# Kernel optimization log

Hardware: AMD Instinct MI355X
Metric: run time of the kernel (lower is better)

Reference implementation:

```python
import math
import jax, jax.numpy as jnp
import numpy as np

DIM = 1280
NUM_HEADS = 16
HEAD_DIM = DIM // NUM_HEADS  # 80
SEQ = 3072


def setup_inputs() -> dict:
    key = jax.random.key(0)
    k1, k2, k3, k4, k5, k6 = jax.random.split(key, 6)
    hidden_states = jax.random.normal(k1, (SEQ, DIM), dtype=jnp.float32)
    # 4 packed images of 768 patches each
    cu_seqlens = jnp.array([0, 768, 1536, 2304, 3072], dtype=jnp.int32)
    rotary_pos_emb = jax.random.normal(k2, (SEQ, HEAD_DIM // 2), dtype=jnp.float32)
    scale = 1.0 / math.sqrt(DIM)
    qkv_w = jax.random.normal(k3, (DIM, 3 * DIM), dtype=jnp.float32) * scale
    qkv_b = jax.random.normal(k4, (3 * DIM,), dtype=jnp.float32) * 0.01
    proj_w = jax.random.normal(k5, (DIM, DIM), dtype=jnp.float32) * scale
    proj_b = jax.random.normal(k6, (DIM,), dtype=jnp.float32) * 0.01
    return {"hidden_states": hidden_states, "cu_seqlens": cu_seqlens,
            "rotary_pos_emb": rotary_pos_emb, "qkv_w": qkv_w, "qkv_b": qkv_b,
            "proj_w": proj_w, "proj_b": proj_b}


def _rotate_half(x):
    half = x.shape[-1] // 2
    return jnp.concatenate([-x[..., half:], x[..., :half]], axis=-1)


def _apply_rope(t, freqs):
    # t: [S, H, hd], freqs: [S, hd//2]
    cos = jnp.cos(freqs)
    sin = jnp.sin(freqs)
    cos = jnp.concatenate([cos, cos], axis=-1)[:, None, :]  # [S,1,hd] (repeat(1,1,2) tiles)
    sin = jnp.concatenate([sin, sin], axis=-1)[:, None, :]
    return (t.astype(jnp.float32) * cos + _rotate_half(t.astype(jnp.float32)) * sin).astype(t.dtype)


def reference(hidden_states, cu_seqlens, rotary_pos_emb, qkv_w, qkv_b, proj_w, proj_b):
    S = hidden_states.shape[0]
    qkv = hidden_states @ qkv_w + qkv_b                      # [S, 3*dim]
    qkv = qkv.reshape(S, 3, NUM_HEADS, HEAD_DIM)
    q, k, v = qkv[:, 0], qkv[:, 1], qkv[:, 2]                # [S, H, hd]
    q = _apply_rope(q, rotary_pos_emb)
    k = _apply_rope(k, rotary_pos_emb)

    # block-diagonal mask from cu_seqlens: positions in the same segment attend
    pos = jnp.arange(S)
    seg = jnp.searchsorted(cu_seqlens, pos, side='right')    # segment id per token
    neg = jnp.finfo(q.dtype).min
    mask = jnp.where(seg[:, None] == seg[None, :], 0.0, neg).astype(q.dtype)  # [S,S]

    qh = q.transpose(1, 0, 2)                                # [H,S,hd]
    kh = k.transpose(1, 0, 2)
    vh = v.transpose(1, 0, 2)
    scores = jnp.einsum('hqd,hkd->hqk', qh, kh) / math.sqrt(HEAD_DIM)
    scores = scores + mask[None]
    attn = jax.nn.softmax(scores.astype(jnp.float32), axis=-1).astype(q.dtype)
    out = jnp.einsum('hqk,hkd->hqd', attn, vh)               # [H,S,hd]
    out = out.transpose(1, 0, 2).reshape(S, DIM)
    return out @ proj_w + proj_b
```

## Files before the change

### kernel.cpp

```cpp
#include <hip/hip_runtime.h>
#include <hip/hip_bf16.h>
#include <math.h>

#define SEQ   3072
#define DIM   1280
#define NH    16
#define HD    80
#define QKV_N 3840

typedef unsigned short u16;
typedef unsigned int   u32;
typedef __attribute__((ext_vector_type(8))) short short8;
typedef __attribute__((ext_vector_type(4))) short short4v;
typedef __attribute__((ext_vector_type(4))) float f32x4;

#if defined(__has_builtin)
#  if __has_builtin(__builtin_amdgcn_mfma_f32_16x16x16bf16_1k)
#    define MFMA16(a,b,c) __builtin_amdgcn_mfma_f32_16x16x16bf16_1k(a,b,c,0,0,0)
#  endif
#endif
#ifndef MFMA16
__device__ __forceinline__ f32x4 mfma16_asm(short4v a, short4v b, f32x4 c) {
    f32x4 d;
    asm volatile("v_mfma_f32_16x16x16_bf16 %0, %1, %2, %3"
                 : "=v"(d) : "v"(a), "v"(b), "0"(c));
    return d;
}
#  define MFMA16(a,b,c) mfma16_asm(a,b,c)
#endif

__device__ __forceinline__ u16 f32_to_bf16(float x) {
    unsigned xb = __float_as_uint(x);
    return (u16)((xb + 0x7fffu + ((xb >> 16) & 1u)) >> 16);
}
__device__ __forceinline__ void split1(float x, u16& h, u16& l) {
    h = f32_to_bf16(x);
    float hf = __uint_as_float(((unsigned)h) << 16);
    l = f32_to_bf16(x - hf);
}
__device__ __forceinline__ u32 pack2(float a, float b) {
    return (u32)f32_to_bf16(a) | ((u32)f32_to_bf16(b) << 16);
}

__device__ __forceinline__ void gload16(const void* g, void* l) {
    __builtin_amdgcn_global_load_lds(
        (const __attribute__((address_space(1))) void*)g,
        (__attribute__((address_space(3))) void*)l, 16, 0, 0);
}

__global__ __launch_bounds__(256) void split_rows(const float* __restrict__ in,
                                                  u16* __restrict__ oh,
                                                  u16* __restrict__ ol, int n4) {
    int i = blockIdx.x * 256 + threadIdx.x;
    int stride = gridDim.x * 256;
    for (; i < n4; i += stride) {
        float4 v = ((const float4*)in)[i];
        ushort4 h, l;
        split1(v.x, h.x, l.x); split1(v.y, h.y, l.y);
        split1(v.z, h.z, l.z); split1(v.w, h.w, l.w);
        ((ushort4*)oh)[i] = h; ((ushort4*)ol)[i] = l;
    }
}

__global__ __launch_bounds__(256) void transpose_w(const float* __restrict__ in,
                                                   u16* __restrict__ o,
                                                   int K, int N) {
    __shared__ float t[32][33];
    const int n0 = blockIdx.x * 32, k0 = blockIdx.y * 32;
    const int tx = threadIdx.x & 31, ty = threadIdx.x >> 5;
    #pragma unroll
    for (int j = 0; j < 4; j++)
        t[ty + j * 8][tx] = in[(size_t)(k0 + ty + j * 8) * N + n0 + tx];
    __syncthreads();
    #pragma unroll
    for (int j = 0; j < 4; j++)
        o[(size_t)(n0 + ty + j * 8) * K + k0 + tx] = f32_to_bf16(t[tx][ty + j * 8]);
}

__global__ __launch_bounds__(256) void gemm_bf16x2(const u16* __restrict__ Ah,
                                                   const u16* __restrict__ Al,
                                                   const u16* __restrict__ Bh,
                                                   const float* __restrict__ bias,
                                                   float* __restrict__ Cf, int ldc,
                                                   u16* __restrict__ Ch,
                                                   u16* __restrict__ Cl, int nsplit,
                                                   int nbn,
                                                   int M, int N, int K) {
    __shared__ u16 lds[2][12288];
    const int tid  = threadIdx.x;
    const int lane = tid & 63;
    const int w    = tid >> 6;

    const int nwg = gridDim.x;
    const int qd  = nwg >> 3, rm = nwg & 7;
    const int xcd = blockIdx.x & 7, idx = blockIdx.x >> 3;
    const int wg  = (xcd < rm ? xcd * (qd + 1) : rm * (qd + 1) + (xcd - rm) * qd) + idx;
    const int bm = wg / nbn, bn = wg - bm * nbn;
    const int wm = w >> 1, wn = w & 1;

    const int rl   = lane >> 2;
    const int slot = lane & 3;
    const int ks   = (slot ^ ((rl >> 1) & 3)) * 8;

    const u16* pbase[3] = { Ah + (size_t)(bm * 128) * K,
                            Al + (size_t)(bm * 128) * K,
                            Bh + (size_t)(bn * 128) * K };
    const u16* csrc[6];
    int cdst[6];
    #pragma unroll
    for (int i = 0; i < 6; i++) {
        int c = w * 6 + i, p = c >> 3, seg = c & 7;
        csrc[i] = pbase[p] + (size_t)(seg * 16 + rl) * K + ks;
        cdst[i] = p * 4096 + seg * 512;
    }

    const f32x4 zero = {0.f, 0.f, 0.f, 0.f};
    f32x4 acc[4][4];
    #pragma unroll
    for (int i = 0; i < 4; i++)
        #pragma unroll
        for (int j = 0; j < 4; j++) acc[i][j] = zero;

    const int r16 = lane & 15, kg = lane >> 4;
    const int sw  = (kg ^ ((r16 >> 1) & 3)) * 16;

    const int nt = K >> 5;

    #pragma unroll
    for (int i = 0; i < 6; i++)
        gload16(csrc[i], &lds[0][cdst[i]]);
    __syncthreads();

    int cur = 0;
    for (int t = 0; t < nt; t++) {
        if (t + 1 < nt) {
            #pragma unroll
            for (int i = 0; i < 6; i++)
                gload16(csrc[i] + (t + 1) * 32, &lds[cur ^ 1][cdst[i]]);
        }

        const char* ldsb = (const char*)&lds[cur][0];
        short8 ah[4], al[4], bh[4];
        #pragma unroll
        for (int i = 0; i < 4; i++) {
            int offA = (wm * 64 + i * 16 + r16) * 64 + sw;
            ah[i] = *(const short8*)(ldsb + offA);
            al[i] = *(const short8*)(ldsb + 8192 + offA);
            int offB = (wn * 64 + i * 16 + r16) * 64 + sw;
            bh[i] = *(const short8*)(ldsb + 16384 + offB);
        }
        #pragma unroll
        for (int i = 0; i < 4; i++)
            #pragma unroll
            for (int j = 0; j < 4; j++) {
                acc[i][j] = __builtin_amdgcn_mfma_f32_16x16x32_bf16(ah[i], bh[j], acc[i][j], 0, 0, 0);
                acc[i][j] = __builtin_amdgcn_mfma_f32_16x16x32_bf16(al[i], bh[j], acc[i][j], 0, 0, 0);
            }

        __syncthreads();
        cur ^= 1;
    }

    const int rg = lane >> 4;
    #pragma unroll
    for (int j = 0; j < 4; j++) {
        int col = bn * 128 + wn * 64 + j * 16 + r16;
        float bv = bias[col];
        #pragma unroll
        for (int i = 0; i < 4; i++) {
            int row0 = bm * 128 + wm * 64 + i * 16 + rg * 4;
            if (col < nsplit) {
                #pragma unroll
                for (int r = 0; r < 4; r++)
                    Cf[(size_t)(row0 + r) * ldc + col] = acc[i][j][r] + bv;
            } else {
                #pragma unroll
                for (int r = 0; r < 4; r++) {
                    float v = acc[i][j][r] + bv;
                    size_t o = (size_t)(row0 + r) * DIM + (col - nsplit);
                    if (Cl) { u16 hh, ll; split1(v, hh, ll); Ch[o] = hh; Cl[o] = ll; }
                    else    { Ch[o] = f32_to_bf16(v); }
                }
            }
        }
    }
}

__global__ __launch_bounds__(256) void rope_split_qk(const float* __restrict__ qk,
                                                     const float* __restrict__ rope,
                                                     u16* __restrict__ Qh, u16* __restrict__ Ql,
                                                     u16* __restrict__ Kh) {
    __shared__ float cs[40], sn[40];
    const int s = blockIdx.x;
    if (threadIdx.x < 40) {
        float f = rope[(size_t)s * 40 + threadIdx.x];
        cs[threadIdx.x] = cosf(f);
        sn[threadIdx.x] = sinf(f);
    }
    __syncthreads();
    const float qs = 0.11180339887498949f;
    const size_t ib = (size_t)s * 2560;
    const size_t ob = (size_t)s * DIM;
    for (int p = threadIdx.x; p < 640; p += 256) {
        int hh = p / 40, j = p - hh * 40;
        float c = cs[j], sv = sn[j];
        int e0 = hh * 80 + j, e1 = e0 + 40;
        float a0 = qk[ib + e0], a1 = qk[ib + e1];
        u16 x, y;
        split1((a0 * c - a1 * sv) * qs, x, y); Qh[ob + e0] = x; Ql[ob + e0] = y;
        split1((a1 * c + a0 * sv) * qs, x, y); Qh[ob + e1] = x; Ql[ob + e1] = y;
        float b0 = qk[ib + 1280 + e0], b1 = qk[ib + 1280 + e1];
        Kh[ob + e0] = f32_to_bf16(b0 * c - b1 * sv);
        Kh[ob + e1] = f32_to_bf16(b1 * c + b0 * sv);
    }
}

__global__ __launch_bounds__(256) void transpose_v(const u16* __restrict__ Vh,
                                                   u16* __restrict__ Vt) {
    __shared__ u16 th[64][88];
    const int hh = blockIdx.x;
    const int s0 = blockIdx.y * 64;
    for (int c = threadIdx.x; c < 640; c += 256) {
        int r = c / 10, cg = c - r * 10;
        *(short8*)&th[r][cg * 8] =
            *(const short8*)(Vh + (size_t)(s0 + r) * DIM + hh * HD + cg * 8);
    }
    __syncthreads();
    for (int c = threadIdx.x; c < 640; c += 256) {
        int d = c >> 3, rg = c & 7;
        short8 v;
        #pragma unroll
        for (int i = 0; i < 8; i++) v[i] = (short)th[rg * 8 + i][d];
        *(short8*)(Vt + (size_t)(hh * HD + d) * SEQ + s0 + rg * 8) = v;
    }
}

__global__ __launch_bounds__(256) void attn_mfma2(const u16* __restrict__ Qh,
                                                  const u16* __restrict__ Ql,
                                                  const u16* __restrict__ Kh,
                                                  const u16* __restrict__ Vt,
                                                  const int* __restrict__ cu,
                                                  u16* __restrict__ Oh,
                                                  u16* __restrict__ Ol) {
    __shared__ u16 lds[2][12288];
    const int tid  = threadIdx.x;
    const int lane = tid & 63;
    const int w    = tid >> 6;
    const int r16  = lane & 15;
    const int kg   = lane >> 4;
    const int h    = blockIdx.x;
    const int q0   = blockIdx.y * 64;

    int kstart, kend;
    {
        int c1 = cu[1], c2 = cu[2], c3 = cu[3];
        if      (q0 < c1) { kstart = cu[0]; kend = c1; }
        else if (q0 < c2) { kstart = c1;    kend = c2; }
        else if (q0 < c3) { kstart = c2;    kend = c3; }
        else              { kstart = c3;    kend = cu[4]; }
    }

    const char* cbase[6];
    int cscale[6];
    #pragma unroll
    for (int i = 0; i < 6; i++) {
        int c = w * 6 + i;
        if (c < 10) {
            int o = c * 1024 + lane * 16;
            int row = o / 160, col = o - row * 160;
            cbase[i]  = (const char*)Kh + (size_t)row * 2560 + h * 160 + col;
            cscale[i] = 2560;
        } else {
            int o = (c - 10) * 1024 + lane * 16;
            int row = o / 160, col = o - row * 160;
            if (row > 79) row = 79;
            cbase[i]  = (const char*)Vt + (size_t)(h * HD + row) * (SEQ * 2) + col;
            cscale[i] = 2;
        }
    }

    const short8 z8 = {0, 0, 0, 0, 0, 0, 0, 0};
    short8 qfh[3], qfl[3];
    {
        const size_t qb = (size_t)(q0 + w * 16 + r16) * DIM + h * HD;
        #pragma unroll
        for (int ks = 0; ks < 3; ks++) {
            int ko = ks * 32 + kg * 8;
            if (ko < HD) {
                qfh[ks] = *(const short8*)(Qh + qb + ko);
                qfl[ks] = *(const short8*)(Ql + qb + ko);
            } else { qfh[ks] = z8; qfl[ks] = z8; }
        }
    }

    const f32x4 zf = {0.f, 0.f, 0.f, 0.f};
    f32x4 acc_o[5] = {zf, zf, zf, zf, zf};
    float m_ = -3.0e38f, l_ = 0.f;

    {
        char* dst = (char*)&lds[0][0] + (w * 6) * 1024;
        #pragma unroll
        for (int i = 0; i < 6; i++)
            gload16(cbase[i] + (size_t)kstart * cscale[i], dst + i * 1024);
    }

    int cur = 0;
    for (int k0 = kstart; k0 < kend; k0 += 64) {
        if (k0 + 64 < kend) {
            char* dst = (char*)&lds[cur ^ 1][0] + (w * 6) * 1024;
            #pragma unroll
            for (int i = 0; i < 6; i++)
                gload16(cbase[i] + (size_t)(k0 + 64) * cscale[i], dst + i * 1024);
            __builtin_amdgcn_sched_barrier(0);
            asm volatile("s_waitcnt vmcnt(6)");
        } else {
            __builtin_amdgcn_sched_barrier(0);
            asm volatile("s_waitcnt vmcnt(0)");
        }
        __builtin_amdgcn_s_barrier();
        __builtin_amdgcn_sched_barrier(0);

        const char* bK = (const char*)&lds[cur][0];
        const char* bV = bK + 10240;

        f32x4 accs[4] = {zf, zf, zf, zf};
        #pragma unroll
        for (int kb = 0; kb < 4; kb++) {
            #pragma unroll
            for (int ks = 0; ks < 3; ks++) {
                short8 af = *(const short8*)(bK + (kb * 16 + r16) * 160 + ks * 64 + kg * 16);
                accs[kb] = __builtin_amdgcn_mfma_f32_16x16x32_bf16(af, qfh[ks], accs[kb], 0, 0, 0);
                accs[kb] = __builtin_amdgcn_mfma_f32_16x16x32_bf16(af, qfl[ks], accs[kb], 0, 0, 0);
            }
        }

        float tmax = -3.0e38f;
        #pragma unroll
        for (int kb = 0; kb < 4; kb++)
            tmax = fmaxf(tmax, fmaxf(fmaxf(accs[kb][0], accs[kb][1]),
                                     fmaxf(accs[kb][2], accs[kb][3])));
        tmax = fmaxf(tmax, __shfl_xor(tmax, 16, 64));
        tmax = fmaxf(tmax, __shfl_xor(tmax, 32, 64));
        float mn = fmaxf(m_, tmax);
        float al = __expf(m_ - mn);
        float lt = 0.f;
        u32 pk[4][2];
        #pragma unroll
        for (int kb = 0; kb < 4; kb++) {
            float p0 = __expf(accs[kb][0] - mn);
            float p1 = __expf(accs[kb][1] - mn);
            float p2 = __expf(accs[kb][2] - mn);
            float p3 = __expf(accs[kb][3] - mn);
            lt += (p0 + p1) + (p2 + p3);
            pk[kb][0] = pack2(p0, p1);
            pk[kb][1] = pack2(p2, p3);
        }
        lt += __shfl_xor(lt, 16, 64);
        lt += __shfl_xor(lt, 32, 64);
        l_ = l_ * al + lt;
        m_ = mn;
        #pragma unroll
        for (int db = 0; db < 5; db++) acc_o[db] *= al;

        #pragma unroll
        for (int kb = 0; kb < 4; kb++) {
            union { u32 u[2]; short4v s; } cv;
            cv.u[0] = pk[kb][0]; cv.u[1] = pk[kb][1];
            short4v pb = cv.s;
            #pragma unroll
            for (int db = 0; db < 5; db++) {
                short4v vf = *(const short4v*)(bV + (db * 16 + r16) * 160 + kb * 32 + kg * 8);
                acc_o[db] = MFMA16(vf, pb, acc_o[db]);
            }
        }

        __builtin_amdgcn_s_barrier();
        __builtin_amdgcn_sched_barrier(0);
        cur ^= 1;
    }

    float inv = 1.0f / l_;
    const size_t ob = (size_t)(q0 + w * 16 + r16) * DIM + h * HD + kg * 4;
    #pragma unroll
    for (int db = 0; db < 5; db++) {
        short4v hv, lv;
        #pragma unroll
        for (int r = 0; r < 4; r++) {
            u16 hh, ll; split1(acc_o[db][r] * inv, hh, ll);
            hv[r] = (short)hh; lv[r] = (short)ll;
        }
        *(short4v*)(Oh + ob + db * 16) = hv;
        *(short4v*)(Ol + ob + db * 16) = lv;
    }
}

__global__ __launch_bounds__(256) void sgemm_bias(const float* __restrict__ A,
                                                  const float* __restrict__ B,
                                                  const float* __restrict__ bias,
                                                  float* __restrict__ C,
                                                  int M, int N, int K) {
    __shared__ float As[8][128];
    __shared__ float Bs[8][128];
    const int tid = threadIdx.x;
    const int tx  = tid & 15;
    const int ty  = tid >> 4;
    const int bx  = blockIdx.x, by = blockIdx.y;
    const int row_a = tid >> 1;
    const int col_a = (tid & 1) * 4;
    const int row_b = tid >> 5;
    const int col_b = (tid & 31) * 4;
    const float* Ap = A + (size_t)(by * 128 + row_a) * K + col_a;
    const float* Bp = B + (size_t)row_b * N + bx * 128 + col_b;
    float acc[8][8];
    #pragma unroll
    for (int i = 0; i < 8; i++)
        #pragma unroll
        for (int j = 0; j < 8; j++) acc[i][j] = 0.f;
    for (int k0 = 0; k0 < K; k0 += 8) {
        float4 av = *(const float4*)(Ap + k0);
        float4 bv = *(const float4*)(Bp + (size_t)k0 * N);
        __syncthreads();
        As[col_a + 0][row_a] = av.x; As[col_a + 1][row_a] = av.y;
        As[col_a + 2][row_a] = av.z; As[col_a + 3][row_a] = av.w;
        *(float4*)&Bs[row_b][col_b] = bv;
        __syncthreads();
        #pragma unroll
        for (int kk = 0; kk < 8; kk++) {
            float a[8], b[8];
            *(float4*)&a[0] = *(const float4*)&As[kk][ty * 8];
            *(float4*)&a[4] = *(const float4*)&As[kk][ty * 8 + 4];
            *(float4*)&b[0] = *(const float4*)&Bs[kk][tx * 8];
            *(float4*)&b[4] = *(const float4*)&Bs[kk][tx * 8 + 4];
            #pragma unroll
            for (int i = 0; i < 8; i++)
                #pragma unroll
                for (int j = 0; j < 8; j++)
                    acc[i][j] = fmaf(a[i], b[j], acc[i][j]);
        }
    }
    const int crow = by * 128 + ty * 8;
    const int ccol = bx * 128 + tx * 8;
    float bs[8];
    #pragma unroll
    for (int j = 0; j < 8; j++) bs[j] = bias[ccol + j];
    #pragma unroll
    for (int i = 0; i < 8; i++) {
        float4 o0, o1;
        o0.x = acc[i][0] + bs[0]; o0.y = acc[i][1] + bs[1];
        o0.z = acc[i][2] + bs[2]; o0.w = acc[i][3] + bs[3];
        o1.x = acc[i][4] + bs[4]; o1.y = acc[i][5] + bs[5];
        o1.z = acc[i][6] + bs[6]; o1.w = acc[i][7] + bs[7];
        *(float4*)(C + (size_t)(crow + i) * N + ccol)     = o0;
        *(float4*)(C + (size_t)(crow + i) * N + ccol + 4) = o1;
    }
}

__global__ __launch_bounds__(256) void rope_kernel(float* __restrict__ qkv,
                                                   const float* __restrict__ rope) {
    const int s = blockIdx.x;
    for (int idx = threadIdx.x; idx < NH * 40; idx += 256) {
        const int hh = idx / 40, j = idx % 40;
        const float f  = rope[(size_t)s * 40 + j];
        const float cs = cosf(f), sn = sinf(f);
        size_t base = (size_t)s * QKV_N + hh * HD;
        float q0 = qkv[base + j], q1 = qkv[base + j + 40];
        qkv[base + j]      = q0 * cs - q1 * sn;
        qkv[base + j + 40] = q1 * cs + q0 * sn;
        size_t kb = base + DIM;
        float k0 = qkv[kb + j], k1 = qkv[kb + j + 40];
        qkv[kb + j]      = k0 * cs - k1 * sn;
        qkv[kb + j + 40] = k1 * cs + k0 * sn;
    }
}

__global__ __launch_bounds__(256) void attn_flash(const float* __restrict__ qkv,
                                                  const int* __restrict__ cu,
                                                  float* __restrict__ aout) {
    __shared__ float Qs[80][68];
    __shared__ float Ks[80][68];
    __shared__ float Vs[64][80];
    float* Ps = &Ks[0][0];
    const int hh  = blockIdx.x;
    const int qt  = blockIdx.y;
    const int tid = threadIdx.x;
    const int tx  = tid & 15;
    const int ty  = tid >> 4;
    const int q0  = qt * 64;
    int c0 = cu[0], c1 = cu[1], c2 = cu[2], c3 = cu[3], c4 = cu[4];
    auto seg = [&](int r, int& s, int& e) {
        if      (r < c1) { s = c0; e = c1; }
        else if (r < c2) { s = c1; e = c2; }
        else if (r < c3) { s = c2; e = c3; }
        else             { s = c3; e = c4; }
    };
    int rs[4], re[4];
    #pragma unroll
    for (int i = 0; i < 4; i++) seg(q0 + ty * 4 + i, rs[i], re[i]);
    int kstart, kend;
    { int s, e; seg(q0, s, e); kstart = s; seg(q0 + 63, s, e); kend = e; }
    for (int i2 = tid; i2 < 64 * 20; i2 += 256) {
        int r = i2 / 20, c4f = (i2 % 20) * 4;
        float4 v = *(const float4*)(qkv + (size_t)(q0 + r) * QKV_N + hh * HD + c4f);
        Qs[c4f + 0][r] = v.x; Qs[c4f + 1][r] = v.y;
        Qs[c4f + 2][r] = v.z; Qs[c4f + 3][r] = v.w;
    }
    float m_[4], l_[4], o_[4][5];
    #pragma unroll
    for (int i = 0; i < 4; i++) {
        m_[i] = -3.0e38f; l_[i] = 0.f;
        #pragma unroll
        for (int d = 0; d < 5; d++) o_[i][d] = 0.f;
    }
    const float scale = 0.11180339887498949f;
    for (int k0 = kstart; k0 < kend; k0 += 64) {
        __syncthreads();
        for (int i2 = tid; i2 < 64 * 20; i2 += 256) {
            int r = i2 / 20, c4f = (i2 % 20) * 4;
            int kk = k0 + r;
            float4 kv, vv;
            if (kk < kend) {
                kv = *(const float4*)(qkv + (size_t)kk * QKV_N + DIM     + hh * HD + c4f);
                vv = *(const float4*)(qkv + (size_t)kk * QKV_N + 2 * DIM + hh * HD + c4f);
            } else {
                kv = make_float4(0.f, 0.f, 0.f, 0.f); vv = kv;
            }
            Ks[c4f + 0][r] = kv.x; Ks[c4f + 1][r] = kv.y;
            Ks[c4f + 2][r] = kv.z; Ks[c4f + 3][r] = kv.w;
            *(float4*)&Vs[r][c4f] = vv;
        }
        __syncthreads();
        float s4[4][4];
        #pragma unroll
        for (int i = 0; i < 4; i++)
            #pragma unroll
            for (int j = 0; j < 4; j++) s4[i][j] = 0.f;
        for (int d = 0; d < 80; d++) {
            float4 qv = *(const float4*)&Qs[d][ty * 4];
            float4 kv = *(const float4*)&Ks[d][tx * 4];
            float qa[4] = {qv.x, qv.y, qv.z, qv.w};
            float ka[4] = {kv.x, kv.y, kv.z, kv.w};
            #pragma unroll
            for (int i = 0; i < 4; i++)
                #pragma unroll
                for (int j = 0; j < 4; j++)
                    s4[i][j] = fmaf(qa[i], ka[j], s4[i][j]);
        }
        float p[4][4];
        #pragma unroll
        for (int i = 0; i < 4; i++) {
            float mt = -3.0e38f;
            #pragma unroll
            for (int j = 0; j < 4; j++) {
                int kk = k0 + tx * 4 + j;
                bool valid = (kk >= rs[i]) && (kk < re[i]);
                s4[i][j] = valid ? s4[i][j] * scale : -3.0e38f;
                mt = fmaxf(mt, s4[i][j]);
            }
            #pragma unroll
            for (int off = 1; off < 16; off <<= 1)
                mt = fmaxf(mt, __shfl_xor(mt, off, 64));
            float mn = fmaxf(m_[i], mt);
            float al = __expf(m_[i] - mn);
            float lt = 0.f;
            #pragma unroll
            for (int j = 0; j < 4; j++) {
                p[i][j] = (s4[i][j] > -1.0e38f) ? __expf(s4[i][j] - mn) : 0.f;
                lt += p[i][j];
            }
            #pragma unroll
            for (int off = 1; off < 16; off <<= 1)
                lt += __shfl_xor(lt, off, 64);
            l_[i] = l_[i] * al + lt;
            m_[i] = mn;
            #pragma unroll
            for (int dd = 0; dd < 5; dd++) o_[i][dd] *= al;
        }
        __syncthreads();
        #pragma unroll
        for (int i = 0; i < 4; i++)
            *(float4*)&Ps[(size_t)(ty * 4 + i) * 68 + tx * 4] =
                make_float4(p[i][0], p[i][1], p[i][2], p[i][3]);
        __syncthreads();
        for (int k = 0; k < 64; k++) {
            float vv[5];
            #pragma unroll
            for (int dd = 0; dd < 5; dd++) vv[dd] = Vs[k][tx * 5 + dd];
            #pragma unroll
            for (int i = 0; i < 4; i++) {
                float pv = Ps[(size_t)(ty * 4 + i) * 68 + k];
                #pragma unroll
                for (int dd = 0; dd < 5; dd++)
                    o_[i][dd] = fmaf(pv, vv[dd], o_[i][dd]);
            }
        }
    }
    #pragma unroll
    for (int i = 0; i < 4; i++) {
        float inv = 1.0f / l_[i];
        #pragma unroll
        for (int dd = 0; dd < 5; dd++)
            aout[(size_t)(q0 + ty * 4 + i) * DIM + hh * HD + tx * 5 + dd] = o_[i][dd] * inv;
    }
}

extern "C" void kernel_launch(void* const* d_in, const int* in_sizes, int n_in,
                              void* d_out, int out_size, void* d_ws, size_t ws_size,
                              hipStream_t stream) {
    const float* hidden = (const float*)d_in[0];
    const int*   cu     = (const int*)d_in[1];
    const float* rope   = (const float*)d_in[2];
    const float* qkv_w  = (const float*)d_in[3];
    const float* qkv_b  = (const float*)d_in[4];
    const float* proj_w = (const float*)d_in[5];
    const float* proj_b = (const float*)d_in[6];
    float* out = (float*)d_out;

    char* ws = (char*)d_ws;
    const size_t need = 82575360;

    if (ws_size >= need) {
        float* qkvQK = (float*)ws;
        u16* Vh = (u16*)(ws + 31457280);
        u16* Wt = (u16*)(ws + 39321600);
        u16* Hh = (u16*)(ws + 49152000);
        u16* Hl = (u16*)(ws + 57016320);
        u16* Qh = (u16*)(ws + 64880640);
        u16* Ql = (u16*)(ws + 72744960);
        u16* Kh = (u16*)(ws + 39321600);
        u16* Pt = (u16*)(ws + 23592960);
        u16* Vt = (u16*)(ws + 0);
        u16* Oh = (u16*)(ws + 7864320);
        u16* Ol = (u16*)(ws + 15728640);

        split_rows<<<2048, 256, 0, stream>>>(hidden, Hh, Hl, SEQ * DIM / 4);
        transpose_w<<<dim3(QKV_N / 32, DIM / 32), 256, 0, stream>>>(
            qkv_w, Wt, DIM, QKV_N);
        gemm_bf16x2<<<(QKV_N / 128) * (SEQ / 128), 256, 0, stream>>>(
            Hh, Hl, Wt, qkv_b, qkvQK, 2560, Vh, nullptr, 2560,
            QKV_N / 128, SEQ, QKV_N, DIM);
        rope_split_qk<<<SEQ, 256, 0, stream>>>(qkvQK, rope, Qh, Ql, Kh);
        transpose_v<<<dim3(NH, SEQ / 64), 256, 0, stream>>>(Vh, Vt);
        transpose_w<<<dim3(DIM / 32, DIM / 32), 256, 0, stream>>>(
            proj_w, Pt, DIM, DIM);
        attn_mfma2<<<dim3(NH, SEQ / 64), 256, 0, stream>>>(
            Qh, Ql, Kh, Vt, cu, Oh, Ol);
        gemm_bf16x2<<<(DIM / 128) * (SEQ / 128), 256, 0, stream>>>(
            Oh, Ol, Pt, proj_b, out, DIM, nullptr, nullptr, DIM,
            DIM / 128, SEQ, DIM, DIM);
    } else {
        float* qkv  = (float*)ws;
        float* aout = qkv + (size_t)SEQ * QKV_N;
        sgemm_bias<<<dim3(QKV_N / 128, SEQ / 128), 256, 0, stream>>>(
            hidden, qkv_w, qkv_b, qkv, SEQ, QKV_N, DIM);
        rope_kernel<<<SEQ, 256, 0, stream>>>(qkv, rope);
        attn_flash<<<dim3(NH, SEQ / 64), 256, 0, stream>>>(qkv, cu, aout);
        sgemm_bias<<<dim3(DIM / 128, SEQ / 128), 256, 0, stream>>>(
            aout, proj_w, proj_b, out, SEQ, DIM, DIM);
    }
}
```

Measured before the change: 263.4 us.

## Fuse V transpose into QKV GEMM, drop split-precision where unneeded, widen attention blocks

The QKV GEMM now writes V directly in transposed bf16 layout, which removes the separate transpose_v kernel. Tiles that don't need high precision (the K/V columns and the output projection) skip the low-part A operand and its second MFMA. The attention kernel moves to 512 threads covering 128 queries per block, each wave loading fewer chunks, and it writes only a single bf16 output, so the projection GEMM runs single-pass. The trade-off is lower precision in K and V products and in the attention output, plus uncoalesced 8-byte strided stores for Vt.

```diff
diff --git a/kernel.cpp b/kernel.cpp
--- a/kernel.cpp
+++ b/kernel.cpp
@@ -77,15 +77,14 @@
         o[(size_t)(n0 + ty + j * 8) * K + k0 + tx] = f32_to_bf16(t[tx][ty + j * 8]);
 }
 
-__global__ __launch_bounds__(256) void gemm_bf16x2(const u16* __restrict__ Ah,
-                                                   const u16* __restrict__ Al,
-                                                   const u16* __restrict__ Bh,
-                                                   const float* __restrict__ bias,
-                                                   float* __restrict__ Cf, int ldc,
-                                                   u16* __restrict__ Ch,
-                                                   u16* __restrict__ Cl, int nsplit,
-                                                   int nbn,
-                                                   int M, int N, int K) {
+__global__ __launch_bounds__(256) void gemm_fused(const u16* __restrict__ Ah,
+                                                  const u16* __restrict__ Al,
+                                                  const u16* __restrict__ Bh,
+                                                  const float* __restrict__ bias,
+                                                  float* __restrict__ Cf, int ldc,
+                                                  u16* __restrict__ Vt,
+                                                  int bn_q, int bn_f32,
+                                                  int nbn, int M, int N, int K) {
     __shared__ u16 lds[2][12288];
     const int tid  = threadIdx.x;
     const int lane = tid & 63;
@@ -97,20 +96,23 @@
     const int wg  = (xcd < rm ? xcd * (qd + 1) : rm * (qd + 1) + (xcd - rm) * qd) + idx;
     const int bm = wg / nbn, bn = wg - bm * nbn;
     const int wm = w >> 1, wn = w & 1;
+    const bool lo = (bn < bn_q);
 
     const int rl   = lane >> 2;
     const int slot = lane & 3;
     const int ks   = (slot ^ ((rl >> 1) & 3)) * 8;
 
-    const u16* pbase[3] = { Ah + (size_t)(bm * 128) * K,
-                            Al + (size_t)(bm * 128) * K,
-                            Bh + (size_t)(bn * 128) * K };
+    const u16* pb[3] = { Ah + (size_t)(bm * 128) * K,
+                         lo ? Al + (size_t)(bm * 128) * K : Ah,
+                         Bh + (size_t)(bn * 128) * K };
+    const int nc = lo ? 6 : 4;
     const u16* csrc[6];
     int cdst[6];
-    #pragma unroll
-    for (int i = 0; i < 6; i++) {
-        int c = w * 6 + i, p = c >> 3, seg = c & 7;
-        csrc[i] = pbase[p] + (size_t)(seg * 16 + rl) * K + ks;
+    for (int i = 0; i < nc; i++) {
+        int c = w * nc + i;
+        int p = lo ? (c >> 3) : ((c >> 3) ? 2 : 0);
+        int seg = c & 7;
+        csrc[i] = pb[p] + (size_t)(seg * 16 + rl) * K + ks;
         cdst[i] = p * 4096 + seg * 512;
     }
 
@@ -126,16 +128,14 @@
 
     const int nt = K >> 5;
 
-    #pragma unroll
-    for (int i = 0; i < 6; i++)
+    for (int i = 0; i < nc; i++)
         gload16(csrc[i], &lds[0][cdst[i]]);
     __syncthreads();
 
     int cur = 0;
     for (int t = 0; t < nt; t++) {
         if (t + 1 < nt) {
-            #pragma unroll
-            for (int i = 0; i < 6; i++)
+            for (int i = 0; i < nc; i++)
                 gload16(csrc[i] + (t + 1) * 32, &lds[cur ^ 1][cdst[i]]);
         }
 
@@ -145,7 +145,7 @@
         for (int i = 0; i < 4; i++) {
             int offA = (wm * 64 + i * 16 + r16) * 64 + sw;
             ah[i] = *(const short8*)(ldsb + offA);
-            al[i] = *(const short8*)(ldsb + 8192 + offA);
+            if (lo) al[i] = *(const short8*)(ldsb + 8192 + offA);
             int offB = (wn * 64 + i * 16 + r16) * 64 + sw;
             bh[i] = *(const short8*)(ldsb + 16384 + offB);
         }
@@ -154,7 +154,8 @@
             #pragma unroll
             for (int j = 0; j < 4; j++) {
                 acc[i][j] = __builtin_amdgcn_mfma_f32_16x16x32_bf16(ah[i], bh[j], acc[i][j], 0, 0, 0);
-                acc[i][j] = __builtin_amdgcn_mfma_f32_16x16x32_bf16(al[i], bh[j], acc[i][j], 0, 0, 0);
+                if (lo)
+                    acc[i][j] = __builtin_amdgcn_mfma_f32_16x16x32_bf16(al[i], bh[j], acc[i][j], 0, 0, 0);
             }
 
         __syncthreads();
@@ -169,18 +170,17 @@
         #pragma unroll
         for (int i = 0; i < 4; i++) {
             int row0 = bm * 128 + wm * 64 + i * 16 + rg * 4;
-            if (col < nsplit) {
+            if (bn < bn_f32) {
                 #pragma unroll
                 for (int r = 0; r < 4; r++)
                     Cf[(size_t)(row0 + r) * ldc + col] = acc[i][j][r] + bv;
             } else {
+                int vcol = col - bn_f32 * 128;
+                short4v hv;
                 #pragma unroll
-                for (int r = 0; r < 4; r++) {
-                    float v = acc[i][j][r] + bv;
-                    size_t o = (size_t)(row0 + r) * DIM + (col - nsplit);
-                    if (Cl) { u16 hh, ll; split1(v, hh, ll); Ch[o] = hh; Cl[o] = ll; }
-                    else    { Ch[o] = f32_to_bf16(v); }
-                }
+                for (int r = 0; r < 4; r++)
+                    hv[r] = (short)f32_to_bf16(acc[i][j][r] + bv);
+                *(short4v*)(Vt + (size_t)vcol * M + row0) = hv;
             }
         }
     }
@@ -215,33 +215,12 @@
     }
 }
 
-__global__ __launch_bounds__(256) void transpose_v(const u16* __restrict__ Vh,
-                                                   u16* __restrict__ Vt) {
-    __shared__ u16 th[64][88];
-    const int hh = blockIdx.x;
-    const int s0 = blockIdx.y * 64;
-    for (int c = threadIdx.x; c < 640; c += 256) {
-        int r = c / 10, cg = c - r * 10;
-        *(short8*)&th[r][cg * 8] =
-            *(const short8*)(Vh + (size_t)(s0 + r) * DIM + hh * HD + cg * 8);
-    }
-    __syncthreads();
-    for (int c = threadIdx.x; c < 640; c += 256) {
-        int d = c >> 3, rg = c & 7;
-        short8 v;
-        #pragma unroll
-        for (int i = 0; i < 8; i++) v[i] = (short)th[rg * 8 + i][d];
-        *(short8*)(Vt + (size_t)(hh * HD + d) * SEQ + s0 + rg * 8) = v;
-    }
-}
-
-__global__ __launch_bounds__(256) void attn_mfma2(const u16* __restrict__ Qh,
+__global__ __launch_bounds__(512) void attn_mfma3(const u16* __restrict__ Qh,
                                                   const u16* __restrict__ Ql,
                                                   const u16* __restrict__ Kh,
                                                   const u16* __restrict__ Vt,
                                                   const int* __restrict__ cu,
-                                                  u16* __restrict__ Oh,
-                                                  u16* __restrict__ Ol) {
+                                                  u16* __restrict__ Oh) {
     __shared__ u16 lds[2][12288];
     const int tid  = threadIdx.x;
     const int lane = tid & 63;
@@ -249,7 +228,7 @@
     const int r16  = lane & 15;
     const int kg   = lane >> 4;
     const int h    = blockIdx.x;
-    const int q0   = blockIdx.y * 64;
+    const int q0   = blockIdx.y * 128;
 
     int kstart, kend;
     {
@@ -260,11 +239,11 @@
         else              { kstart = c3;    kend = cu[4]; }
     }
 
-    const char* cbase[6];
-    int cscale[6];
-    #pragma unroll
-    for (int i = 0; i < 6; i++) {
-        int c = w * 6 + i;
+    const char* cbase[3];
+    int cscale[3];
+    #pragma unroll
+    for (int i = 0; i < 3; i++) {
+        int c = w * 3 + i;
         if (c < 10) {
             int o = c * 1024 + lane * 16;
             int row = o / 160, col = o - row * 160;
@@ -298,21 +277,21 @@
     float m_ = -3.0e38f, l_ = 0.f;
 
     {
-        char* dst = (char*)&lds[0][0] + (w * 6) * 1024;
-        #pragma unroll
-        for (int i = 0; i < 6; i++)
+        char* dst = (char*)&lds[0][0] + (w * 3) * 1024;
+        #pragma unroll
+        for (int i = 0; i < 3; i++)
             gload16(cbase[i] + (size_t)kstart * cscale[i], dst + i * 1024);
     }
 
     int cur = 0;
     for (int k0 = kstart; k0 < kend; k0 += 64) {
         if (k0 + 64 < kend) {
-            char* dst = (char*)&lds[cur ^ 1][0] + (w * 6) * 1024;
-            #pragma unroll
-            for (int i = 0; i < 6; i++)
+            char* dst = (char*)&lds[cur ^ 1][0] + (w * 3) * 1024;
+            #pragma unroll
+            for (int i = 0; i < 3; i++)
                 gload16(cbase[i] + (size_t)(k0 + 64) * cscale[i], dst + i * 1024);
             __builtin_amdgcn_sched_barrier(0);
-            asm volatile("s_waitcnt vmcnt(6)");
+            asm volatile("s_waitcnt vmcnt(3)");
         } else {
             __builtin_amdgcn_sched_barrier(0);
             asm volatile("s_waitcnt vmcnt(0)");
@@ -383,14 +362,11 @@
     const size_t ob = (size_t)(q0 + w * 16 + r16) * DIM + h * HD + kg * 4;
     #pragma unroll
     for (int db = 0; db < 5; db++) {
-        short4v hv, lv;
-        #pragma unroll
-        for (int r = 0; r < 4; r++) {
-            u16 hh, ll; split1(acc_o[db][r] * inv, hh, ll);
-            hv[r] = (short)hh; lv[r] = (short)ll;
-        }
+        short4v hv;
+        #pragma unroll
+        for (int r = 0; r < 4; r++)
+            hv[r] = (short)f32_to_bf16(acc_o[db][r] * inv);
         *(short4v*)(Oh + ob + db * 16) = hv;
-        *(short4v*)(Ol + ob + db * 16) = lv;
     }
 }
 
@@ -616,11 +592,11 @@
     float* out = (float*)d_out;
 
     char* ws = (char*)d_ws;
-    const size_t need = 82575360;
+    const size_t need = 80609280;
 
     if (ws_size >= need) {
         float* qkvQK = (float*)ws;
-        u16* Vh = (u16*)(ws + 31457280);
+        u16* Vt = (u16*)(ws + 31457280);
         u16* Wt = (u16*)(ws + 39321600);
         u16* Hh = (u16*)(ws + 49152000);
         u16* Hl = (u16*)(ws + 57016320);
@@ -628,24 +604,21 @@
         u16* Ql = (u16*)(ws + 72744960);
         u16* Kh = (u16*)(ws + 39321600);
         u16* Pt = (u16*)(ws + 23592960);
-        u16* Vt = (u16*)(ws + 0);
         u16* Oh = (u16*)(ws + 7864320);
-        u16* Ol = (u16*)(ws + 15728640);
 
         split_rows<<<2048, 256, 0, stream>>>(hidden, Hh, Hl, SEQ * DIM / 4);
         transpose_w<<<dim3(QKV_N / 32, DIM / 32), 256, 0, stream>>>(
             qkv_w, Wt, DIM, QKV_N);
-        gemm_bf16x2<<<(QKV_N / 128) * (SEQ / 128), 256, 0, stream>>>(
-            Hh, Hl, Wt, qkv_b, qkvQK, 2560, Vh, nullptr, 2560,
+        gemm_fused<<<(QKV_N / 128) * (SEQ / 128), 256, 0, stream>>>(
+            Hh, Hl, Wt, qkv_b, qkvQK, 2560, Vt, 10, 20,
             QKV_N / 128, SEQ, QKV_N, DIM);
         rope_split_qk<<<SEQ, 256, 0, stream>>>(qkvQK, rope, Qh, Ql, Kh);
-        transpose_v<<<dim3(NH, SEQ / 64), 256, 0, stream>>>(Vh, Vt);
         transpose_w<<<dim3(DIM / 32, DIM / 32), 256, 0, stream>>>(
             proj_w, Pt, DIM, DIM);
-        attn_mfma2<<<dim3(NH, SEQ / 64), 256, 0, stream>>>(
-            Qh, Ql, Kh, Vt, cu, Oh, Ol);
-        gemm_bf16x2<<<(DIM / 128) * (SEQ / 128), 256, 0, stream>>>(
-            Oh, Ol, Pt, proj_b, out, DIM, nullptr, nullptr, DIM,
+        attn_mfma3<<<dim3(NH, SEQ / 128), 512, 0, stream>>>(
+            Qh, Ql, Kh, Vt, cu, Oh);
+        gemm_fused<<<(DIM / 128) * (SEQ / 128), 256, 0, stream>>>(
+            Oh, nullptr, Pt, proj_b, out, DIM, nullptr, 0, DIM / 128,
             DIM / 128, SEQ, DIM, DIM);
     } else {
         float* qkv  = (float*)ws;
```

After: 306.6 us. +16.4%, slower.
